# Optimization experiments

Measured on AMD Instinct MI355X. Metric: run time of the kernel, lower is better.

## Reference

```python
import jax, jax.numpy as jnp
import numpy as np

# Static hyperparameters matching init_kwargs
G, N, D = 8, 8, 8          # groups, filters/group, kernel depth (c = G*D, o = G*N)
W, KS = 16, 4              # kernel width (time window), time stride
AH, AS = 2, 2              # activate_height, activate_stride (freq box-sum window)
C, F = 64, 128             # input channels, embedding (freq bins)
O = G * N                  # out_channels


def setup_inputs() -> dict:
    key = jax.random.key(0)
    kx, kw = jax.random.split(key)
    x = jax.random.normal(kx, (16, C, F, 256), dtype=jnp.float32)
    # xavier-uniform for weight (o, d, e, w)
    fan_in = D * F * W
    fan_out = fan_in  # torch xavier on 4D: fan computed over receptive field; bound below matches scale
    bound = float(np.sqrt(6.0 / (fan_in + fan_out)))
    weight = jax.random.uniform(kw, (O, D, F, W), dtype=jnp.float32, minval=-bound, maxval=bound)
    return {"x": x, "weight": weight}


def reference(x, weight):
    b, c, f, T = x.shape
    t = (T - W) // KS + 1
    # unfold time: x[..., ti*KS + wi] -> [b, c, f, t, W]
    idx = jnp.arange(t)[:, None] * KS + jnp.arange(W)[None, :]
    xu = x[..., idx]
    # split channels (g d) row-major, matching einops 'b (g d) f t w'
    xg = xu.reshape(b, G, D, f, t, W)
    wg = weight.reshape(G, N, D, f, W)
    # fused: multiply-broadcast then sum over d and w (the ones-kernel conv sums
    # over depth d and full width w); height window handled below.
    z = jnp.einsum('bgdftw,gndfw->btgnf', xg, wg)  # [b, t, G, N, f]
    z = z.reshape(b, t, O, f)
    # box-sum over freq with window AH, stride AS ('valid')
    fp = (f - AH) // AS + 1
    pidx = jnp.arange(fp)[:, None] * AS + jnp.arange(AH)
    y = z[..., pidx].sum(-1)  # [b, t, O, fp]
    return jnp.transpose(y, (0, 2, 3, 1))  # [b, O, fp, t]
```

## Files before the change

### kernel.cpp

```cpp
#include <hip/hip_runtime.h>


namespace {
constexpr int kB  = 16;
constexpr int kC  = 64;
constexpr int kF  = 128;
constexpr int kT  = 256;
constexpr int kG  = 8;
constexpr int kD  = 8;
constexpr int kN  = 8;
constexpr int kW  = 16;
constexpr int kKS = 4;
constexpr int kNT = 61;
constexpr int kO  = 64;
constexpr int kFP = 64;
constexpr int kWStride = kD * kF * kW;
}

__global__ __launch_bounds__(256, 2)
void lc2d_kernel(const float* __restrict__ x,
                 const float* __restrict__ wt,
                 float* __restrict__ out) {
  __shared__ float4 wlds[512];

  const int tid  = threadIdx.x;
  const int lane = tid & 63;
  const int wq   = tid >> 6;
  const int fi   = blockIdx.x;
  const int g    = blockIdx.y;

  {
    const float* wb = wt + ((size_t)(g * kN) * kD * kF + (size_t)fi * 2) * kW;
#pragma unroll
    for (int r = 0; r < 2; ++r) {
      const int q  = tid + r * 256;
      const int n  = q >> 6;
      const int dd = (q >> 3) & 7;
      const int fr = (q >> 2) & 1;
      const int qq = q & 3;
      const float* src =
          wb + (size_t)n * kWStride + dd * (kF * kW) + fr * kW + qq * 4;
      wlds[q] = *(const float4*)src;
    }
  }

  const int tc   = (lane < kNT - 1) ? lane : (kNT - 1);
  const int tau0 = tc * kKS;

  const float* xb[4];
#pragma unroll
  for (int bb = 0; bb < 4; ++bb) {
    const int b = wq * 4 + bb;
    xb[bb] = x + (((size_t)b * kC + g * kD) * kF + fi * 2) * kT + tau0;
  }

  float acc[4][kN];
#pragma unroll
  for (int bb = 0; bb < 4; ++bb)
#pragma unroll
    for (int n = 0; n < kN; ++n) acc[bb][n] = 0.f;

  float4 cur[4][4];
#pragma unroll
  for (int bb = 0; bb < 4; ++bb)
#pragma unroll
    for (int q = 0; q < 4; ++q) cur[bb][q] = ((const float4*)xb[bb])[q];

  __syncthreads();

#pragma unroll 2
  for (int it = 0; it < 16; ++it) {
    const int nx = (it < 15) ? it + 1 : 15;
    const size_t roff = ((size_t)(nx >> 1) * kF + (nx & 1)) * kT;
    float4 pre[4][4];
#pragma unroll
    for (int bb = 0; bb < 4; ++bb) {
      const float* xr = xb[bb] + roff;
#pragma unroll
      for (int q = 0; q < 4; ++q) pre[bb][q] = ((const float4*)xr)[q];
    }

    const int qb = it * 4;
    float4 w0 = wlds[qb + 0];
    float4 w1 = wlds[qb + 1];
    float4 w2 = wlds[qb + 2];
    float4 w3 = wlds[qb + 3];
#pragma unroll
    for (int n = 0; n < kN; ++n) {
      float4 nw0, nw1, nw2, nw3;
      if (n < kN - 1) {
        const int qn = qb + (n + 1) * 64;
        nw0 = wlds[qn + 0];
        nw1 = wlds[qn + 1];
        nw2 = wlds[qn + 2];
        nw3 = wlds[qn + 3];
      }
#pragma unroll
      for (int bb = 0; bb < 4; ++bb) {
        float a = acc[bb][n];
        a = fmaf(cur[bb][0].x, w0.x, a);
        a = fmaf(cur[bb][0].y, w0.y, a);
        a = fmaf(cur[bb][0].z, w0.z, a);
        a = fmaf(cur[bb][0].w, w0.w, a);
        a = fmaf(cur[bb][1].x, w1.x, a);
        a = fmaf(cur[bb][1].y, w1.y, a);
        a = fmaf(cur[bb][1].z, w1.z, a);
        a = fmaf(cur[bb][1].w, w1.w, a);
        a = fmaf(cur[bb][2].x, w2.x, a);
        a = fmaf(cur[bb][2].y, w2.y, a);
        a = fmaf(cur[bb][2].z, w2.z, a);
        a = fmaf(cur[bb][2].w, w2.w, a);
        a = fmaf(cur[bb][3].x, w3.x, a);
        a = fmaf(cur[bb][3].y, w3.y, a);
        a = fmaf(cur[bb][3].z, w3.z, a);
        a = fmaf(cur[bb][3].w, w3.w, a);
        acc[bb][n] = a;
      }
      if (n < kN - 1) {
        w0 = nw0; w1 = nw1; w2 = nw2; w3 = nw3;
      }
    }

#pragma unroll
    for (int bb = 0; bb < 4; ++bb)
#pragma unroll
      for (int q = 0; q < 4; ++q) cur[bb][q] = pre[bb][q];
  }

  if (lane < kNT) {
    const size_t s = (size_t)kFP * kNT;
#pragma unroll
    for (int bb = 0; bb < 4; ++bb) {
      const int b = wq * 4 + bb;
      float* ob = out + (((size_t)b * kO + g * kN) * kFP + fi) * (size_t)kNT + lane;
#pragma unroll
      for (int n = 0; n < kN; ++n) ob[(size_t)n * s] = acc[bb][n];
    }
  }
}

extern "C" void kernel_launch(void* const* d_in, const int* in_sizes, int n_in,
                              void* d_out, int out_size, void* d_ws, size_t ws_size,
                              hipStream_t stream) {
  const float* x  = (const float*)d_in[0];
  const float* wt = (const float*)d_in[1];
  float* out      = (float*)d_out;

  dim3 grid(kFP, kG, 1);
  lc2d_kernel<<<grid, 256, 0, stream>>>(x, wt, out);
}
```

Before: 204.0 us.

## Split time window across half-waves and add grid z for more parallelism

Each wave now splits the 16-wide time window into two halves, one per half-wave of 32 lanes. The two halves are combined with a cross-lane shuffle, and each half writes 4 of the 8 filter outputs. The time axis is split over two blocks along grid z, doubling the block count, and launch bounds are raised to 3 blocks per CU. This halves the per-thread register footprint and work so occupancy can rise, at the cost of an extra shuffle reduction and some duplicated edge-lane work.

```diff
diff --git a/kernel.cpp b/kernel.cpp
--- a/kernel.cpp
+++ b/kernel.cpp
@@ -17,7 +17,7 @@
 constexpr int kWStride = kD * kF * kW;
 }
 
-__global__ __launch_bounds__(256, 2)
+__global__ __launch_bounds__(256, 3)
 void lc2d_kernel(const float* __restrict__ x,
                  const float* __restrict__ wt,
                  float* __restrict__ out) {
@@ -26,8 +26,11 @@
   const int tid  = threadIdx.x;
   const int lane = tid & 63;
   const int wq   = tid >> 6;
+  const int tl   = lane & 31;
+  const int th   = lane >> 5;
   const int fi   = blockIdx.x;
   const int g    = blockIdx.y;
+  const int tz   = blockIdx.z;
 
   {
     const float* wb = wt + ((size_t)(g * kN) * kD * kF + (size_t)fi * 2) * kW;
@@ -44,8 +47,9 @@
     }
   }
 
-  const int tc   = (lane < kNT - 1) ? lane : (kNT - 1);
-  const int tau0 = tc * kKS;
+  const int tg = tz * 32 + tl;
+  const int tc = (tg < kNT) ? tl : (kNT - 1 - 32);
+  const int tau0 = (tz * 32 + tc) * kKS + th * 8;
 
   const float* xb[4];
 #pragma unroll
@@ -60,11 +64,11 @@
 #pragma unroll
     for (int n = 0; n < kN; ++n) acc[bb][n] = 0.f;
 
-  float4 cur[4][4];
+  float4 cur[4][2];
 #pragma unroll
   for (int bb = 0; bb < 4; ++bb)
 #pragma unroll
-    for (int q = 0; q < 4; ++q) cur[bb][q] = ((const float4*)xb[bb])[q];
+    for (int q = 0; q < 2; ++q) cur[bb][q] = ((const float4*)xb[bb])[q];
 
   __syncthreads();
 
@@ -72,29 +76,19 @@
   for (int it = 0; it < 16; ++it) {
     const int nx = (it < 15) ? it + 1 : 15;
     const size_t roff = ((size_t)(nx >> 1) * kF + (nx & 1)) * kT;
-    float4 pre[4][4];
+    float4 pre[4][2];
 #pragma unroll
     for (int bb = 0; bb < 4; ++bb) {
       const float* xr = xb[bb] + roff;
 #pragma unroll
-      for (int q = 0; q < 4; ++q) pre[bb][q] = ((const float4*)xr)[q];
+      for (int q = 0; q < 2; ++q) pre[bb][q] = ((const float4*)xr)[q];
     }
 
-    const int qb = it * 4;
-    float4 w0 = wlds[qb + 0];
-    float4 w1 = wlds[qb + 1];
-    float4 w2 = wlds[qb + 2];
-    float4 w3 = wlds[qb + 3];
+    const float4* wrow = &wlds[it * 4 + th * 2];
 #pragma unroll
     for (int n = 0; n < kN; ++n) {
-      float4 nw0, nw1, nw2, nw3;
-      if (n < kN - 1) {
-        const int qn = qb + (n + 1) * 64;
-        nw0 = wlds[qn + 0];
-        nw1 = wlds[qn + 1];
-        nw2 = wlds[qn + 2];
-        nw3 = wlds[qn + 3];
-      }
+      const float4 w0 = wrow[n * 64];
+      const float4 w1 = wrow[n * 64 + 1];
 #pragma unroll
       for (int bb = 0; bb < 4; ++bb) {
         float a = acc[bb][n];
@@ -106,35 +100,32 @@
         a = fmaf(cur[bb][1].y, w1.y, a);
         a = fmaf(cur[bb][1].z, w1.z, a);
         a = fmaf(cur[bb][1].w, w1.w, a);
-        a = fmaf(cur[bb][2].x, w2.x, a);
-        a = fmaf(cur[bb][2].y, w2.y, a);
-        a = fmaf(cur[bb][2].z, w2.z, a);
-        a = fmaf(cur[bb][2].w, w2.w, a);
-        a = fmaf(cur[bb][3].x, w3.x, a);
-        a = fmaf(cur[bb][3].y, w3.y, a);
-        a = fmaf(cur[bb][3].z, w3.z, a);
-        a = fmaf(cur[bb][3].w, w3.w, a);
         acc[bb][n] = a;
-      }
-      if (n < kN - 1) {
-        w0 = nw0; w1 = nw1; w2 = nw2; w3 = nw3;
       }
     }
 
 #pragma unroll
     for (int bb = 0; bb < 4; ++bb)
 #pragma unroll
-      for (int q = 0; q < 4; ++q) cur[bb][q] = pre[bb][q];
+      for (int q = 0; q < 2; ++q) cur[bb][q] = pre[bb][q];
   }
 
-  if (lane < kNT) {
+#pragma unroll
+  for (int bb = 0; bb < 4; ++bb)
+#pragma unroll
+    for (int n = 0; n < kN; ++n)
+      acc[bb][n] += __shfl_xor(acc[bb][n], 32);
+
+  if (tg < kNT) {
     const size_t s = (size_t)kFP * kNT;
+    const int nb = th * 4;
 #pragma unroll
     for (int bb = 0; bb < 4; ++bb) {
       const int b = wq * 4 + bb;
-      float* ob = out + (((size_t)b * kO + g * kN) * kFP + fi) * (size_t)kNT + lane;
+      float* ob =
+          out + (((size_t)b * kO + g * kN + nb) * kFP + fi) * (size_t)kNT + tg;
 #pragma unroll
-      for (int n = 0; n < kN; ++n) ob[(size_t)n * s] = acc[bb][n];
+      for (int j = 0; j < 4; ++j) ob[(size_t)j * s] = acc[bb][nb + j];
     }
   }
 }
@@ -146,6 +137,6 @@
   const float* wt = (const float*)d_in[1];
   float* out      = (float*)d_out;
 
-  dim3 grid(kFP, kG, 1);
+  dim3 grid(kFP, kG, 2);
   lc2d_kernel<<<grid, 256, 0, stream>>>(x, wt, out);
 }
```

Result: slower. 231.4 us (+13.4%).
